# Kernel tuning notes

Measured on AMD Instinct MI355X. Metric: run time of the kernel, lower is better.

The kernel has to match this reference:

```python
import jax, jax.numpy as jnp
import numpy as np

DIM = 2048
N_HEADS = 16
Q_RANK = 1536
KV_RANK = 512
D_NOPE = 128
D_ROPE = 64
D_V = 128
EPS = 1e-6
B, S = 2, 2048
ROPE_THETA = 10000.0


def rmsnorm(x, w, eps=EPS):
    return x * jax.lax.rsqrt(jnp.mean(x * x, axis=-1, keepdims=True) + eps) * w


def apply_rope(x):
    # x: [b, h, s, d] with d even; LLaMA-style interleaved pair rotation
    b, h, s, d = x.shape
    inv_freq = 1.0 / (ROPE_THETA ** (jnp.arange(0, d, 2, dtype=jnp.float32) / d))
    ang = jnp.arange(s, dtype=jnp.float32)[:, None] * inv_freq[None, :]  # [s, d/2]
    cos, sin = jnp.cos(ang), jnp.sin(ang)
    xr = x.reshape(b, h, s, d // 2, 2)
    x1, x2 = xr[..., 0], xr[..., 1]
    o1 = x1 * cos - x2 * sin
    o2 = x1 * sin + x2 * cos
    return jnp.stack([o1, o2], axis=-1).reshape(b, h, s, d)


def setup_inputs() -> dict:
    key = jax.random.key(0)
    ks = jax.random.split(key, 10)
    std = 0.02
    return {
        "x": jax.random.normal(ks[0], (B, S, DIM), dtype=jnp.float32),
        "wq_down": jax.random.normal(ks[1], (Q_RANK, DIM), dtype=jnp.float32) * std,
        "q_norm_w": jnp.ones((Q_RANK,), dtype=jnp.float32),
        "wq_up": jax.random.normal(ks[2], (N_HEADS * D_NOPE, Q_RANK), dtype=jnp.float32) * std,
        "wq_rope": jax.random.normal(ks[3], (N_HEADS * D_ROPE, Q_RANK), dtype=jnp.float32) * std,
        "wkv_down": jax.random.normal(ks[4], (KV_RANK, DIM), dtype=jnp.float32) * std,
        "kv_norm_w": jnp.ones((KV_RANK,), dtype=jnp.float32),
        "wkv_up": jax.random.normal(ks[5], (N_HEADS * (D_NOPE + D_V), KV_RANK), dtype=jnp.float32) * std,
        "wk_rope": jax.random.normal(ks[6], (D_ROPE, DIM), dtype=jnp.float32) * std,
        "wo": jax.random.normal(ks[7], (DIM, N_HEADS * D_V), dtype=jnp.float32) * std,
    }


def reference(x, wq_down, q_norm_w, wq_up, wq_rope, wkv_down, kv_norm_w, wkv_up, wk_rope, wo):
    bs, s, _ = x.shape
    # low-rank Q path
    q_c = rmsnorm(x @ wq_down.T, q_norm_w)                              # [b,s,qr]
    q_nope = (q_c @ wq_up.T).reshape(bs, s, N_HEADS, D_NOPE).transpose(0, 2, 1, 3)
    q_pe = (q_c @ wq_rope.T).reshape(bs, s, N_HEADS, D_ROPE).transpose(0, 2, 1, 3)
    # low-rank KV path
    kv_c = rmsnorm(x @ wkv_down.T, kv_norm_w)                           # [b,s,kvr]
    kv_up = (kv_c @ wkv_up.T).reshape(bs, s, N_HEADS, D_NOPE + D_V)
    k_nope = kv_up[..., :D_NOPE].transpose(0, 2, 1, 3)                  # [b,h,s,dn]
    v = kv_up[..., D_NOPE:].transpose(0, 2, 1, 3)                       # [b,h,s,dv]
    # shared rope key (1 head), broadcast across heads
    k_rope = (x @ wk_rope.T).reshape(bs, s, 1, D_ROPE).transpose(0, 2, 1, 3)  # [b,1,s,dr]
    q_pe = apply_rope(q_pe)
    k_rope = apply_rope(k_rope)
    q = jnp.concatenate([q_nope, q_pe], axis=-1)                        # [b,h,s,dn+dr]
    k = jnp.concatenate([k_nope, jnp.broadcast_to(k_rope, (bs, N_HEADS, s, D_ROPE))], axis=-1)
    scale = 1.0 / np.sqrt(D_NOPE + D_ROPE)
    scores = jnp.einsum('bhqd,bhkd->bhqk', q, k) * scale                # [b,h,s,s]
    causal = jnp.tril(jnp.ones((s, s), dtype=bool))
    scores = jnp.where(causal, scores, -jnp.inf)
    probs = jax.nn.softmax(scores, axis=-1)
    out = jnp.einsum('bhqk,bhkv->bhqv', probs, v)                       # [b,h,s,dv]
    out = out.transpose(0, 2, 1, 3).reshape(bs, s, N_HEADS * D_V)
    return out @ wo.T
```

## Files before the change

### kernel.cpp

```cpp
#include <hip/hip_runtime.h>
#include <stdint.h>

typedef _Float16 f16x8 __attribute__((ext_vector_type(8)));
typedef _Float16 f16x4 __attribute__((ext_vector_type(4)));
typedef float fx4 __attribute__((ext_vector_type(4)));

static constexpr int S_LEN = 2048;
static constexpr int BATCH = 2;
static constexpr int TOKENS = BATCH * S_LEN;
static constexpr int DIM = 2048;
static constexpr int NH = 16;
static constexpr int QR = 1536;
static constexpr int KVR = 512;
static constexpr int DN = 128;
static constexpr int DR = 64;
static constexpr int DV = 128;

__device__ __forceinline__ void async16(const _Float16* g, _Float16* lds_base_uniform) {
  __builtin_amdgcn_global_load_lds(
      (const __attribute__((address_space(1))) void*)g,
      (__attribute__((address_space(3))) void*)lds_base_uniform, 16, 0, 0);
}

__device__ __forceinline__ void bar() {
  asm volatile("" ::: "memory");
  __builtin_amdgcn_s_barrier();
  asm volatile("" ::: "memory");
}
#define VMWAIT(n) asm volatile("s_waitcnt vmcnt(" #n ")" ::: "memory")

#define ROR16(x, ctrl) \
  __uint_as_float(__builtin_amdgcn_update_dpp(__float_as_uint(x), __float_as_uint(x), \
                                              (ctrl), 0xF, 0xF, false))

struct CvtSegs {
  const float* src[8];
  _Float16* dst[8];
  int n4[8];
  int cum[9];
};
__global__ __launch_bounds__(256) void cvt_all(CvtSegs s) {
  const int b = blockIdx.x;
  int seg = 0;
#pragma unroll
  for (int k = 0; k < 7; ++k) seg += (b >= s.cum[seg + 1]) ? 1 : 0;
  const int i = (b - s.cum[seg]) * 256 + threadIdx.x;
  if (i >= s.n4[seg]) return;
  fx4 v = *(const fx4*)(s.src[seg] + (size_t)i * 4);
  f16x4 o;
  o[0] = (_Float16)v[0]; o[1] = (_Float16)v[1];
  o[2] = (_Float16)v[2]; o[3] = (_Float16)v[3];
  *(f16x4*)(s.dst[seg] + (size_t)i * 4) = o;
}

template <int MODE>
__global__ __launch_bounds__(256) void gemm_nt(const _Float16* __restrict__ A,
                                               const _Float16* __restrict__ W,
                                               void* __restrict__ C0v,
                                               void* __restrict__ C1v,
                                               int M, int N, int K) {
  __shared__ __attribute__((aligned(16))) _Float16 As[3][128 * 32];
  __shared__ __attribute__((aligned(16))) _Float16 Ws[3][128 * 32];
  const int tid = threadIdx.x;
  const int lane = tid & 63;
  const int wave = tid >> 6;
  const int wr = (wave >> 1) * 64;
  const int wc = (wave & 1) * 64;
  const int m16 = lane & 15;
  const int quad = lane >> 4;
  const int m0 = blockIdx.y * 128;
  const int n0 = blockIdx.x * 128;

  auto stage = [&](int buf, int k0) {
#pragma unroll
    for (int p = 0; p < 2; ++p) {
      const int cb = p * 256 + wave * 64;
      const int ch = cb + lane;
      const int r = ch >> 2;
      const int c8 = (ch & 3) * 8;
      async16(A + (size_t)(m0 + r) * K + k0 + c8, &As[buf][cb * 8]);
      async16(W + (size_t)(n0 + r) * K + k0 + c8, &Ws[buf][cb * 8]);
    }
  };

  const fx4 fz = {0.f, 0.f, 0.f, 0.f};
  fx4 acc[4][4];
#pragma unroll
  for (int i = 0; i < 4; ++i)
#pragma unroll
    for (int j = 0; j < 4; ++j) acc[i][j] = fz;

  const int nkt = K >> 5;
  stage(0, 0);
  stage(1, 32);
  int cur = 0;
  for (int kt = 0; kt < nkt; ++kt) {
    if (kt + 1 < nkt) { VMWAIT(4); } else { VMWAIT(0); }
    bar();
    if (kt + 2 < nkt) {
      int b2 = cur + 2; if (b2 >= 3) b2 -= 3;
      stage(b2, (kt + 2) * 32);
    }
    const _Float16* as = As[cur];
    const _Float16* ws = Ws[cur];
    f16x8 af[4], wf[4];
#pragma unroll
    for (int i = 0; i < 4; ++i)
      af[i] = *(const f16x8*)(&as[(wr + i * 16 + m16) * 32 + quad * 8]);
#pragma unroll
    for (int j = 0; j < 4; ++j)
      wf[j] = *(const f16x8*)(&ws[(wc + j * 16 + m16) * 32 + quad * 8]);
#pragma unroll
    for (int i = 0; i < 4; ++i)
#pragma unroll
      for (int j = 0; j < 4; ++j)
        acc[i][j] = __builtin_amdgcn_mfma_f32_16x16x32_f16(af[i], wf[j], acc[i][j], 0, 0, 0);
    if (++cur == 3) cur = 0;
  }

#pragma unroll
  for (int j = 0; j < 4; ++j) {
    const int col = n0 + wc + j * 16 + m16;
    if (MODE == 2) {
      _Float16* KN = (_Float16*)C0v;
      _Float16* VT = (_Float16*)C1v;
      const int head = col >> 8;
      const int sub = col & 255;
      if (sub < 128) {
#pragma unroll
        for (int i = 0; i < 4; ++i)
#pragma unroll
          for (int r = 0; r < 4; ++r)
            KN[(size_t)(m0 + wr + i * 16 + quad * 4 + r) * 2048 + head * 128 + sub] =
                (_Float16)acc[i][j][r];
      } else {
        const int dv = sub - 128;
#pragma unroll
        for (int i = 0; i < 4; ++i) {
          f16x4 v;
#pragma unroll
          for (int r = 0; r < 4; ++r) v[r] = (_Float16)acc[i][j][r];
          *(f16x4*)(&VT[(size_t)(head * 128 + dv) * TOKENS + m0 + wr + i * 16 + quad * 4]) = v;
        }
      }
    } else if (MODE == 3) {
#pragma unroll
      for (int i = 0; i < 4; ++i)
#pragma unroll
        for (int r = 0; r < 4; ++r) {
          const size_t row = (size_t)(m0 + wr + i * 16 + quad * 4 + r);
          if (col < 2048) ((_Float16*)C0v)[row * 2048 + col] = (_Float16)acc[i][j][r];
          else ((_Float16*)C1v)[row * 1024 + col - 2048] = (_Float16)acc[i][j][r];
        }
    } else if (MODE == 4) {
      if (col < 576) {
#pragma unroll
        for (int i = 0; i < 4; ++i)
#pragma unroll
          for (int r = 0; r < 4; ++r) {
            const size_t row = (size_t)(m0 + wr + i * 16 + quad * 4 + r);
            if (col < 512) ((_Float16*)C0v)[row * 512 + col] = (_Float16)acc[i][j][r];
            else ((_Float16*)C1v)[row * 64 + col - 512] = (_Float16)acc[i][j][r];
          }
      }
    } else {
      if (col < N) {
#pragma unroll
        for (int i = 0; i < 4; ++i)
#pragma unroll
          for (int r = 0; r < 4; ++r) {
            const size_t row = (size_t)(m0 + wr + i * 16 + quad * 4 + r);
            if (MODE == 0) ((_Float16*)C0v)[row * N + col] = (_Float16)acc[i][j][r];
            else ((float*)C0v)[row * N + col] = acc[i][j][r];
          }
      }
    }
  }
}

template <int NC>
__global__ __launch_bounds__(256) void rmsnorm_ip(_Float16* __restrict__ xx,
                                                  const float* __restrict__ w) {
  const int row = blockIdx.x;
  _Float16* p = xx + (size_t)row * NC;
  float ss = 0.f;
  for (int c = threadIdx.x; c < NC; c += 256) {
    const float v = (float)p[c];
    ss += v * v;
  }
#pragma unroll
  for (int d = 1; d < 64; d <<= 1) ss += __shfl_xor(ss, d);
  __shared__ float red[4];
  if ((threadIdx.x & 63) == 0) red[threadIdx.x >> 6] = ss;
  __syncthreads();
  const float rs = rsqrtf((red[0] + red[1] + red[2] + red[3]) * (1.0f / NC) + 1e-6f);
  for (int c = threadIdx.x; c < NC; c += 256)
    p[c] = (_Float16)((float)p[c] * rs * w[c]);
}

__global__ void rope_q(_Float16* __restrict__ qpe) {
  const int idx = blockIdx.x * 256 + threadIdx.x;
  const int t = idx >> 9;
  const int rem = idx & 511;
  const int hh = rem >> 5;
  const int i = rem & 31;
  const int s = t & (S_LEN - 1);
  const float fr = exp2f(-(float)i * 0.4152410118609203f);
  const float ang = (float)s * fr;
  const float sn = sinf(ang), cs = cosf(ang);
  const size_t base = (size_t)t * (NH * DR) + hh * DR + 2 * i;
  const float x1 = (float)qpe[base];
  const float x2 = (float)qpe[base + 1];
  qpe[base] = (_Float16)(x1 * cs - x2 * sn);
  qpe[base + 1] = (_Float16)(x1 * sn + x2 * cs);
}

__global__ void rope_k(_Float16* __restrict__ kr) {
  const int idx = blockIdx.x * 256 + threadIdx.x;
  const int t = idx >> 5;
  const int i = idx & 31;
  const int s = t & (S_LEN - 1);
  const float fr = exp2f(-(float)i * 0.4152410118609203f);
  const float ang = (float)s * fr;
  const float sn = sinf(ang), cs = cosf(ang);
  const size_t base = (size_t)t * DR + 2 * i;
  const float x1 = (float)kr[base];
  const float x2 = (float)kr[base + 1];
  kr[base] = (_Float16)(x1 * cs - x2 * sn);
  kr[base + 1] = (_Float16)(x1 * sn + x2 * cs);
}

__global__ __launch_bounds__(256, 2) void mla_attn(
    const _Float16* __restrict__ qn,
    const _Float16* __restrict__ qp,
    const _Float16* __restrict__ kn,
    const _Float16* __restrict__ kr,
    const _Float16* __restrict__ vT,
    _Float16* __restrict__ out)
{
  __shared__ __attribute__((aligned(16))) _Float16 Ks[2][768 * 8];
  __shared__ __attribute__((aligned(16))) _Float16 Vs[2][512 * 8];
  __shared__ __attribute__((aligned(16))) _Float16 Ps[4][16][40];

  const int bid = blockIdx.x;
  const int j = bid >> 5;
  const int bh = bid & 31;
  const int b = bh >> 4;
  const int h = bh & 15;
  const int q32 = 31 - j;
  const int qb = q32 * 64;
  const int tok0 = b * S_LEN;

  const int tid = threadIdx.x;
  const int lane = tid & 63;
  const int wave = tid >> 6;
  const int m16 = lane & 15;
  const int quad = lane >> 4;
  const int R0 = qb + wave * 16;

  auto stageKV = [&](int buf, int kbase) {
#pragma unroll
    for (int jj = 0; jj < 3; ++jj) {
      const int i = wave * 3 + jj;
      const int ch = i * 2 + (lane >> 5);
      const int key = lane & 31;
      const _Float16* g = (ch < 16)
          ? kn + (size_t)(tok0 + kbase + key) * 2048 + h * 128 + ch * 8
          : kr + (size_t)(tok0 + kbase + key) * 64 + (ch - 16) * 8;
      async16(g, &Ks[buf][i * 512]);
    }
#pragma unroll
    for (int jj = 0; jj < 2; ++jj) {
      const int i = wave * 2 + jj;
      const int p = i * 64 + lane;
      const int L = p ^ ((p >> 3) & 3);
      const int dv = L >> 2;
      const int qc = L & 3;
      async16(vT + (size_t)(h * 128 + dv) * TOKENS + tok0 + kbase + qc * 8,
              &Vs[buf][i * 512]);
    }
  };

  const float scale2 = 0.07216878364870323f * 1.4426950408889634f;
  const fx4 fz = {0.f, 0.f, 0.f, 0.f};

  f16x8 qf[6];
  {
    const size_t t = (size_t)(tok0 + qb + wave * 16 + m16);
#pragma unroll
    for (int kk = 0; kk < 4; ++kk)
      qf[kk] = *(const f16x8*)(qn + t * 2048 + h * 128 + kk * 32 + quad * 8);
#pragma unroll
    for (int kk = 0; kk < 2; ++kk)
      qf[4 + kk] = *(const f16x8*)(qp + t * 1024 + h * 64 + kk * 32 + quad * 8);
  }

  fx4 oacc[8];
#pragma unroll
  for (int n = 0; n < 8; ++n) oacc[n] = fz;
  float mst[4], lst[4];
#pragma unroll
  for (int r = 0; r < 4; ++r) { mst[r] = -3.0e38f; lst[r] = 0.f; }

  const int nkt = (qb >> 5) + 2;

  stageKV(0, 0);
  for (int kt = 0; kt < nkt; ++kt) {
    const int kbase = kt * 32;
    __syncthreads();
    if (kt + 1 < nkt) stageKV((kt + 1) & 1, kbase + 32);

    const bool live = (kbase <= R0 + 15);
    if (!live) continue;
    const _Float16* ks = Ks[kt & 1];
    const _Float16* vs = Vs[kt & 1];

    fx4 sc[2];
    sc[0] = fz; sc[1] = fz;
    __builtin_amdgcn_s_setprio(1);
#pragma unroll
    for (int kk = 0; kk < 6; ++kk) {
#pragma unroll
      for (int n = 0; n < 2; ++n) {
        f16x8 kf = *(const f16x8*)(&ks[(kk * 128 + quad * 32 + n * 16 + m16) * 8]);
        sc[n] = __builtin_amdgcn_mfma_f32_16x16x32_f16(qf[kk], kf, sc[n], 0, 0, 0);
      }
    }
    __builtin_amdgcn_s_setprio(0);

    f16x8 vf[8];
#pragma unroll
    for (int n8 = 0; n8 < 8; ++n8) {
      const int c0 = (n8 * 16 + m16) * 4 + quad;
      vf[n8] = *(const f16x8*)(&vs[(c0 ^ ((c0 >> 3) & 3)) * 8]);
    }

    const bool needmask = (kbase + 31 > R0);
    float alpha[4];
    bool any_upd = false;
#pragma unroll
    for (int r = 0; r < 4; ++r) {
      float v0 = sc[0][r] * scale2;
      float v1 = sc[1][r] * scale2;
      if (needmask) {
        const int qrow = R0 + quad * 4 + r;
        if (kbase + m16 > qrow)      v0 = -3.0e38f;
        if (kbase + 16 + m16 > qrow) v1 = -3.0e38f;
      }
      float mx = fmaxf(v0, v1);
      mx = fmaxf(mx, ROR16(mx, 0x128));
      mx = fmaxf(mx, ROR16(mx, 0x124));
      mx = fmaxf(mx, ROR16(mx, 0x122));
      mx = fmaxf(mx, ROR16(mx, 0x121));
      float al = 1.0f;
      if (__any(mx > mst[r] + 10.0f)) {
        const float mn = fmaxf(mst[r], mx);
        al = exp2f(mst[r] - mn);
        mst[r] = mn;
        any_upd = true;
      }
      alpha[r] = al;
      const float p0 = exp2f(v0 - mst[r]);
      const float p1 = exp2f(v1 - mst[r]);
      float ls = p0 + p1;
      ls += ROR16(ls, 0x128);
      ls += ROR16(ls, 0x124);
      ls += ROR16(ls, 0x122);
      ls += ROR16(ls, 0x121);
      lst[r] = lst[r] * al + ls;
      _Float16* pr = &Ps[wave][quad * 4 + r][0];
      pr[m16] = (_Float16)p0;
      pr[16 + m16] = (_Float16)p1;
    }
    if (any_upd) {
#pragma unroll
      for (int n8 = 0; n8 < 8; ++n8)
#pragma unroll
        for (int r = 0; r < 4; ++r) oacc[n8][r] *= alpha[r];
    }

    f16x8 pf = *(const f16x8*)(&Ps[wave][m16][quad * 8]);
    __builtin_amdgcn_s_setprio(1);
#pragma unroll
    for (int n8 = 0; n8 < 8; ++n8)
      oacc[n8] = __builtin_amdgcn_mfma_f32_16x16x32_f16(pf, vf[n8], oacc[n8], 0, 0, 0);
    __builtin_amdgcn_s_setprio(0);
  }

  float inv[4];
#pragma unroll
  for (int r = 0; r < 4; ++r) inv[r] = 1.0f / lst[r];
#pragma unroll
  for (int n8 = 0; n8 < 8; ++n8) {
#pragma unroll
    for (int r = 0; r < 4; ++r) {
      const size_t t = (size_t)(tok0 + qb + wave * 16 + quad * 4 + r);
      out[t * 2048 + h * 128 + n8 * 16 + m16] = (_Float16)(oacc[n8][r] * inv[r]);
    }
  }
}

extern "C" void kernel_launch(void* const* d_in, const int* in_sizes, int n_in,
                              void* d_out, int out_size, void* d_ws, size_t ws_size,
                              hipStream_t stream) {
  const float* x         = (const float*)d_in[0];
  const float* wq_down   = (const float*)d_in[1];
  const float* q_norm_w  = (const float*)d_in[2];
  const float* wq_up     = (const float*)d_in[3];
  const float* wq_rope   = (const float*)d_in[4];
  const float* wkv_down  = (const float*)d_in[5];
  const float* kv_norm_w = (const float*)d_in[6];
  const float* wkv_up    = (const float*)d_in[7];
  const float* wk_rope   = (const float*)d_in[8];
  const float* wo        = (const float*)d_in[9];
  float* out = (float*)d_out;

  char* ws = (char*)d_ws;
  size_t off = 0;
  auto alloc = [&](size_t bytes) {
    char* p = ws + off;
    off += (bytes + 255) & ~(size_t)255;
    return p;
  };
  _Float16* x_h     = (_Float16*)alloc((size_t)TOKENS * DIM * 2);
  _Float16* wqd_h   = (_Float16*)alloc((size_t)QR * DIM * 2);
  _Float16* wquqr_h = (_Float16*)alloc((size_t)3072 * QR * 2);
  _Float16* wkvdr_h = (_Float16*)alloc((size_t)576 * DIM * 2);
  _Float16* wkvu_h  = (_Float16*)alloc((size_t)NH * 256 * KVR * 2);
  _Float16* wo_h    = (_Float16*)alloc((size_t)DIM * NH * DV * 2);
  _Float16* qc_h    = (_Float16*)alloc((size_t)TOKENS * QR * 2);
  _Float16* kvc_h   = (_Float16*)alloc((size_t)TOKENS * KVR * 2);
  _Float16* qnope_h = (_Float16*)alloc((size_t)TOKENS * 2048 * 2);
  _Float16* qpe_h   = (_Float16*)alloc((size_t)TOKENS * 1024 * 2);
  _Float16* knope_h = (_Float16*)alloc((size_t)TOKENS * 2048 * 2);
  _Float16* vT_h    = (_Float16*)alloc((size_t)2048 * TOKENS * 2);
  _Float16* krope_h = (_Float16*)alloc((size_t)TOKENS * DR * 2);
  _Float16* attn_h  = (_Float16*)alloc((size_t)TOKENS * 2048 * 2);

  CvtSegs cs;
  const float* srcs[8] = {x, wq_down, wq_up, wq_rope, wkv_down, wk_rope, wkv_up, wo};
  _Float16* dsts[8] = {x_h, wqd_h, wquqr_h, wquqr_h + (size_t)2048 * QR,
                       wkvdr_h, wkvdr_h + (size_t)512 * DIM, wkvu_h, wo_h};
  const size_t ns[8] = {(size_t)TOKENS * DIM, (size_t)QR * DIM, (size_t)2048 * QR,
                        (size_t)1024 * QR, (size_t)KVR * DIM, (size_t)DR * DIM,
                        (size_t)NH * 256 * KVR, (size_t)DIM * NH * DV};
  int cum = 0;
  for (int i = 0; i < 8; ++i) {
    cs.src[i] = srcs[i];
    cs.dst[i] = dsts[i];
    cs.n4[i] = (int)(ns[i] / 4);
    cs.cum[i] = cum;
    cum += (cs.n4[i] + 255) / 256;
  }
  cs.cum[8] = cum;
  cvt_all<<<dim3(cum), 256, 0, stream>>>(cs);

  auto gx = [](int n) { return (unsigned)((n + 127) / 128); };
  const unsigned gm = TOKENS / 128;

  gemm_nt<0><<<dim3(gx(QR), gm), 256, 0, stream>>>(x_h, wqd_h, qc_h, nullptr, TOKENS, QR, DIM);
  rmsnorm_ip<QR><<<dim3(TOKENS), 256, 0, stream>>>(qc_h, q_norm_w);
  gemm_nt<4><<<dim3(gx(576), gm), 256, 0, stream>>>(x_h, wkvdr_h, kvc_h, krope_h, TOKENS, 576, DIM);
  rmsnorm_ip<KVR><<<dim3(TOKENS), 256, 0, stream>>>(kvc_h, kv_norm_w);
  rope_k<<<dim3(TOKENS * 32 / 256), 256, 0, stream>>>(krope_h);
  gemm_nt<3><<<dim3(gx(3072), gm), 256, 0, stream>>>(qc_h, wquqr_h, qnope_h, qpe_h, TOKENS, 3072, QR);
  rope_q<<<dim3(TOKENS * NH * 32 / 256), 256, 0, stream>>>(qpe_h);
  gemm_nt<2><<<dim3(gx(4096), gm), 256, 0, stream>>>(kvc_h, wkvu_h, knope_h, vT_h, TOKENS, 4096, KVR);
  mla_attn<<<dim3(1024), 256, 0, stream>>>(qnope_h, qpe_h, knope_h, krope_h, vT_h, attn_h);
  gemm_nt<1><<<dim3(gx(DIM), gm), 256, 0, stream>>>(attn_h, wo_h, out, nullptr, TOKENS, DIM, NH * DV);
}
```

Baseline: 512.4 us.

## Merge down-projections, fuse norms and rope, fold q-rope and row-sum into attention

Concatenates the wq_down, wkv_down and wk_rope weights so a single GEMM produces q_c, kv_c and k_rope. The two rmsnorms and rope_k become one launch, and the two up-projection GEMMs become one launch dispatched by block index. The q rope is applied in registers while Q is loaded inside attention, and the softmax denominator is now taken from an extra MFMA against a ones vector instead of DPP reductions; sin/cos use hardware revolution-based intrinsics. This removes several launches and a global read-write pass over q_pe, at the cost of an extra MFMA per tile and lower-precision trig.

```diff
diff --git a/kernel.cpp b/kernel.cpp
--- a/kernel.cpp
+++ b/kernel.cpp
@@ -33,6 +33,13 @@
   __uint_as_float(__builtin_amdgcn_update_dpp(__float_as_uint(x), __float_as_uint(x), \
                                               (ctrl), 0xF, 0xF, false))
 
+__device__ __forceinline__ void sincos_rev(float ang, float* sn, float* cs) {
+  float rev = ang * 0.15915494309189535f;
+  rev -= floorf(rev);
+  *sn = __builtin_amdgcn_sinf(rev);
+  *cs = __builtin_amdgcn_cosf(rev);
+}
+
 struct CvtSegs {
   const float* src[8];
   _Float16* dst[8];
@@ -58,6 +65,7 @@
                                                const _Float16* __restrict__ W,
                                                void* __restrict__ C0v,
                                                void* __restrict__ C1v,
+                                               void* __restrict__ C2v,
                                                int M, int N, int K) {
   __shared__ __attribute__((aligned(16))) _Float16 As[3][128 * 32];
   __shared__ __attribute__((aligned(16))) _Float16 Ws[3][128 * 32];
@@ -121,9 +129,112 @@
 #pragma unroll
   for (int j = 0; j < 4; ++j) {
     const int col = n0 + wc + j * 16 + m16;
-    if (MODE == 2) {
-      _Float16* KN = (_Float16*)C0v;
-      _Float16* VT = (_Float16*)C1v;
+    if (MODE == 5) {
+#pragma unroll
+      for (int i = 0; i < 4; ++i)
+#pragma unroll
+        for (int r = 0; r < 4; ++r) {
+          const size_t row = (size_t)(m0 + wr + i * 16 + quad * 4 + r);
+          const _Float16 v = (_Float16)acc[i][j][r];
+          if (col < 1536)      ((_Float16*)C0v)[row * 1536 + col] = v;
+          else if (col < 2048) ((_Float16*)C1v)[row * 512 + col - 1536] = v;
+          else if (col < 2112) ((_Float16*)C2v)[row * 64 + col - 2048] = v;
+        }
+    } else {
+      if (col < N) {
+#pragma unroll
+        for (int i = 0; i < 4; ++i)
+#pragma unroll
+          for (int r = 0; r < 4; ++r) {
+            const size_t row = (size_t)(m0 + wr + i * 16 + quad * 4 + r);
+            ((float*)C0v)[row * N + col] = acc[i][j][r];
+          }
+      }
+    }
+  }
+}
+
+__global__ __launch_bounds__(256) void gemm_up(
+    const _Float16* __restrict__ qc, const _Float16* __restrict__ wqu,
+    const _Float16* __restrict__ kvc, const _Float16* __restrict__ wkvu,
+    _Float16* __restrict__ qnope, _Float16* __restrict__ qpe,
+    _Float16* __restrict__ knope, _Float16* __restrict__ vT) {
+  __shared__ __attribute__((aligned(16))) _Float16 As[3][128 * 32];
+  __shared__ __attribute__((aligned(16))) _Float16 Ws[3][128 * 32];
+  const int tid = threadIdx.x;
+  const int lane = tid & 63;
+  const int wave = tid >> 6;
+  const int wr = (wave >> 1) * 64;
+  const int wc = (wave & 1) * 64;
+  const int m16 = lane & 15;
+  const int quad = lane >> 4;
+  const int m0 = blockIdx.y * 128;
+  const bool isq = (blockIdx.x < 24);
+  const int n0 = (isq ? blockIdx.x : blockIdx.x - 24) * 128;
+  const _Float16* A = isq ? qc : kvc;
+  const _Float16* W = isq ? wqu : wkvu;
+  const int K = isq ? QR : KVR;
+
+  auto stage = [&](int buf, int k0) {
+#pragma unroll
+    for (int p = 0; p < 2; ++p) {
+      const int cb = p * 256 + wave * 64;
+      const int ch = cb + lane;
+      const int r = ch >> 2;
+      const int c8 = (ch & 3) * 8;
+      async16(A + (size_t)(m0 + r) * K + k0 + c8, &As[buf][cb * 8]);
+      async16(W + (size_t)(n0 + r) * K + k0 + c8, &Ws[buf][cb * 8]);
+    }
+  };
+
+  const fx4 fz = {0.f, 0.f, 0.f, 0.f};
+  fx4 acc[4][4];
+#pragma unroll
+  for (int i = 0; i < 4; ++i)
+#pragma unroll
+    for (int j = 0; j < 4; ++j) acc[i][j] = fz;
+
+  const int nkt = K >> 5;
+  stage(0, 0);
+  stage(1, 32);
+  int cur = 0;
+  for (int kt = 0; kt < nkt; ++kt) {
+    if (kt + 1 < nkt) { VMWAIT(4); } else { VMWAIT(0); }
+    bar();
+    if (kt + 2 < nkt) {
+      int b2 = cur + 2; if (b2 >= 3) b2 -= 3;
+      stage(b2, (kt + 2) * 32);
+    }
+    const _Float16* as = As[cur];
+    const _Float16* ws = Ws[cur];
+    f16x8 af[4], wf[4];
+#pragma unroll
+    for (int i = 0; i < 4; ++i)
+      af[i] = *(const f16x8*)(&as[(wr + i * 16 + m16) * 32 + quad * 8]);
+#pragma unroll
+    for (int j = 0; j < 4; ++j)
+      wf[j] = *(const f16x8*)(&ws[(wc + j * 16 + m16) * 32 + quad * 8]);
+#pragma unroll
+    for (int i = 0; i < 4; ++i)
+#pragma unroll
+      for (int j = 0; j < 4; ++j)
+        acc[i][j] = __builtin_amdgcn_mfma_f32_16x16x32_f16(af[i], wf[j], acc[i][j], 0, 0, 0);
+    if (++cur == 3) cur = 0;
+  }
+
+#pragma unroll
+  for (int j = 0; j < 4; ++j) {
+    const int col = n0 + wc + j * 16 + m16;
+    if (isq) {
+#pragma unroll
+      for (int i = 0; i < 4; ++i)
+#pragma unroll
+        for (int r = 0; r < 4; ++r) {
+          const size_t row = (size_t)(m0 + wr + i * 16 + quad * 4 + r);
+          if (col < 2048) qnope[row * 2048 + col] = (_Float16)acc[i][j][r];
+          else qpe[row * 1024 + col - 2048] = (_Float16)acc[i][j][r];
+        }
+    } else {
       const int head = col >> 8;
       const int sub = col & 255;
       if (sub < 128) {
@@ -131,7 +242,7 @@
         for (int i = 0; i < 4; ++i)
 #pragma unroll
           for (int r = 0; r < 4; ++r)
-            KN[(size_t)(m0 + wr + i * 16 + quad * 4 + r) * 2048 + head * 128 + sub] =
+            knope[(size_t)(m0 + wr + i * 16 + quad * 4 + r) * 2048 + head * 128 + sub] =
                 (_Float16)acc[i][j][r];
       } else {
         const int dv = sub - 128;
@@ -140,94 +251,53 @@
           f16x4 v;
 #pragma unroll
           for (int r = 0; r < 4; ++r) v[r] = (_Float16)acc[i][j][r];
-          *(f16x4*)(&VT[(size_t)(head * 128 + dv) * TOKENS + m0 + wr + i * 16 + quad * 4]) = v;
+          *(f16x4*)(&vT[(size_t)(head * 128 + dv) * TOKENS + m0 + wr + i * 16 + quad * 4]) = v;
         }
       }
-    } else if (MODE == 3) {
-#pragma unroll
-      for (int i = 0; i < 4; ++i)
-#pragma unroll
-        for (int r = 0; r < 4; ++r) {
-          const size_t row = (size_t)(m0 + wr + i * 16 + quad * 4 + r);
-          if (col < 2048) ((_Float16*)C0v)[row * 2048 + col] = (_Float16)acc[i][j][r];
-          else ((_Float16*)C1v)[row * 1024 + col - 2048] = (_Float16)acc[i][j][r];
-        }
-    } else if (MODE == 4) {
-      if (col < 576) {
-#pragma unroll
-        for (int i = 0; i < 4; ++i)
-#pragma unroll
-          for (int r = 0; r < 4; ++r) {
-            const size_t row = (size_t)(m0 + wr + i * 16 + quad * 4 + r);
-            if (col < 512) ((_Float16*)C0v)[row * 512 + col] = (_Float16)acc[i][j][r];
-            else ((_Float16*)C1v)[row * 64 + col - 512] = (_Float16)acc[i][j][r];
-          }
-      }
-    } else {
-      if (col < N) {
-#pragma unroll
-        for (int i = 0; i < 4; ++i)
-#pragma unroll
-          for (int r = 0; r < 4; ++r) {
-            const size_t row = (size_t)(m0 + wr + i * 16 + quad * 4 + r);
-            if (MODE == 0) ((_Float16*)C0v)[row * N + col] = (_Float16)acc[i][j][r];
-            else ((float*)C0v)[row * N + col] = acc[i][j][r];
-          }
-      }
-    }
-  }
-}
-
-template <int NC>
-__global__ __launch_bounds__(256) void rmsnorm_ip(_Float16* __restrict__ xx,
-                                                  const float* __restrict__ w) {
-  const int row = blockIdx.x;
-  _Float16* p = xx + (size_t)row * NC;
-  float ss = 0.f;
-  for (int c = threadIdx.x; c < NC; c += 256) {
-    const float v = (float)p[c];
-    ss += v * v;
-  }
-#pragma unroll
-  for (int d = 1; d < 64; d <<= 1) ss += __shfl_xor(ss, d);
-  __shared__ float red[4];
-  if ((threadIdx.x & 63) == 0) red[threadIdx.x >> 6] = ss;
-  __syncthreads();
-  const float rs = rsqrtf((red[0] + red[1] + red[2] + red[3]) * (1.0f / NC) + 1e-6f);
-  for (int c = threadIdx.x; c < NC; c += 256)
-    p[c] = (_Float16)((float)p[c] * rs * w[c]);
-}
-
-__global__ void rope_q(_Float16* __restrict__ qpe) {
-  const int idx = blockIdx.x * 256 + threadIdx.x;
-  const int t = idx >> 9;
-  const int rem = idx & 511;
-  const int hh = rem >> 5;
-  const int i = rem & 31;
-  const int s = t & (S_LEN - 1);
-  const float fr = exp2f(-(float)i * 0.4152410118609203f);
-  const float ang = (float)s * fr;
-  const float sn = sinf(ang), cs = cosf(ang);
-  const size_t base = (size_t)t * (NH * DR) + hh * DR + 2 * i;
-  const float x1 = (float)qpe[base];
-  const float x2 = (float)qpe[base + 1];
-  qpe[base] = (_Float16)(x1 * cs - x2 * sn);
-  qpe[base + 1] = (_Float16)(x1 * sn + x2 * cs);
-}
-
-__global__ void rope_k(_Float16* __restrict__ kr) {
-  const int idx = blockIdx.x * 256 + threadIdx.x;
-  const int t = idx >> 5;
-  const int i = idx & 31;
-  const int s = t & (S_LEN - 1);
-  const float fr = exp2f(-(float)i * 0.4152410118609203f);
-  const float ang = (float)s * fr;
-  const float sn = sinf(ang), cs = cosf(ang);
-  const size_t base = (size_t)t * DR + 2 * i;
-  const float x1 = (float)kr[base];
-  const float x2 = (float)kr[base + 1];
-  kr[base] = (_Float16)(x1 * cs - x2 * sn);
-  kr[base + 1] = (_Float16)(x1 * sn + x2 * cs);
+    }
+  }
+}
+
+__global__ __launch_bounds__(256) void rms_rope(_Float16* __restrict__ qc,
+                                                const float* __restrict__ qw,
+                                                _Float16* __restrict__ kvc,
+                                                const float* __restrict__ kvw,
+                                                _Float16* __restrict__ kr) {
+  const int bid = blockIdx.x;
+  if (bid < 2 * TOKENS) {
+    const bool isq = bid < TOKENS;
+    const int row = isq ? bid : bid - TOKENS;
+    const int NC = isq ? QR : KVR;
+    _Float16* p = (isq ? qc : kvc) + (size_t)row * NC;
+    const float* w = isq ? qw : kvw;
+    float ss = 0.f;
+    for (int c = threadIdx.x; c < NC; c += 256) {
+      const float v = (float)p[c];
+      ss += v * v;
+    }
+#pragma unroll
+    for (int d = 1; d < 64; d <<= 1) ss += __shfl_xor(ss, d);
+    __shared__ float red[4];
+    if ((threadIdx.x & 63) == 0) red[threadIdx.x >> 6] = ss;
+    __syncthreads();
+    const float rs = rsqrtf((red[0] + red[1] + red[2] + red[3]) / (float)NC + 1e-6f);
+    for (int c = threadIdx.x; c < NC; c += 256)
+      p[c] = (_Float16)((float)p[c] * rs * w[c]);
+  } else {
+    const int idx = (bid - 2 * TOKENS) * 256 + threadIdx.x;
+    const int t = idx >> 5;
+    const int i = idx & 31;
+    const int s = t & (S_LEN - 1);
+    const float fr = exp2f(-(float)i * 0.4152410118609203f);
+    const float ang = (float)s * fr;
+    float sn, cs;
+    sincos_rev(ang, &sn, &cs);
+    const size_t base = (size_t)t * DR + 2 * i;
+    const float x1 = (float)kr[base];
+    const float x2 = (float)kr[base + 1];
+    kr[base] = (_Float16)(x1 * cs - x2 * sn);
+    kr[base + 1] = (_Float16)(x1 * sn + x2 * cs);
+  }
 }
 
 __global__ __launch_bounds__(256, 2) void mla_attn(
@@ -286,21 +356,38 @@
 
   f16x8 qf[6];
   {
-    const size_t t = (size_t)(tok0 + qb + wave * 16 + m16);
+    const int srow = qb + wave * 16 + m16;
+    const size_t t = (size_t)(tok0 + srow);
 #pragma unroll
     for (int kk = 0; kk < 4; ++kk)
       qf[kk] = *(const f16x8*)(qn + t * 2048 + h * 128 + kk * 32 + quad * 8);
 #pragma unroll
-    for (int kk = 0; kk < 2; ++kk)
-      qf[4 + kk] = *(const f16x8*)(qp + t * 1024 + h * 64 + kk * 32 + quad * 8);
-  }
-
-  fx4 oacc[8];
-#pragma unroll
-  for (int n = 0; n < 8; ++n) oacc[n] = fz;
-  float mst[4], lst[4];
-#pragma unroll
-  for (int r = 0; r < 4; ++r) { mst[r] = -3.0e38f; lst[r] = 0.f; }
+    for (int kk = 0; kk < 2; ++kk) {
+      f16x8 v = *(const f16x8*)(qp + t * 1024 + h * 64 + kk * 32 + quad * 8);
+      f16x8 o;
+      const int i0 = kk * 16 + quad * 4;
+#pragma unroll
+      for (int jj = 0; jj < 4; ++jj) {
+        const float ang = (float)srow * exp2f(-(float)(i0 + jj) * 0.4152410118609203f);
+        float sn, cs;
+        sincos_rev(ang, &sn, &cs);
+        const float x1 = (float)v[2 * jj], x2 = (float)v[2 * jj + 1];
+        o[2 * jj]     = (_Float16)(x1 * cs - x2 * sn);
+        o[2 * jj + 1] = (_Float16)(x1 * sn + x2 * cs);
+      }
+      qf[4 + kk] = o;
+    }
+  }
+
+  fx4 oacc[9];
+#pragma unroll
+  for (int n = 0; n < 9; ++n) oacc[n] = fz;
+  float mst[4];
+#pragma unroll
+  for (int r = 0; r < 4; ++r) mst[r] = -3.0e38f;
+  f16x8 vones;
+#pragma unroll
+  for (int e = 0; e < 8; ++e) vones[e] = (_Float16)1.0f;
 
   const int nkt = (qb >> 5) + 2;
 
@@ -347,13 +434,14 @@
         if (kbase + m16 > qrow)      v0 = -3.0e38f;
         if (kbase + 16 + m16 > qrow) v1 = -3.0e38f;
       }
-      float mx = fmaxf(v0, v1);
-      mx = fmaxf(mx, ROR16(mx, 0x128));
-      mx = fmaxf(mx, ROR16(mx, 0x124));
-      mx = fmaxf(mx, ROR16(mx, 0x122));
-      mx = fmaxf(mx, ROR16(mx, 0x121));
+      const float pre = fmaxf(v0, v1);
       float al = 1.0f;
-      if (__any(mx > mst[r] + 10.0f)) {
+      if (__any(pre > mst[r] + 10.0f)) {
+        float mx = pre;
+        mx = fmaxf(mx, ROR16(mx, 0x128));
+        mx = fmaxf(mx, ROR16(mx, 0x124));
+        mx = fmaxf(mx, ROR16(mx, 0x122));
+        mx = fmaxf(mx, ROR16(mx, 0x121));
         const float mn = fmaxf(mst[r], mx);
         al = exp2f(mst[r] - mn);
         mst[r] = mn;
@@ -362,19 +450,13 @@
       alpha[r] = al;
       const float p0 = exp2f(v0 - mst[r]);
       const float p1 = exp2f(v1 - mst[r]);
-      float ls = p0 + p1;
-      ls += ROR16(ls, 0x128);
-      ls += ROR16(ls, 0x124);
-      ls += ROR16(ls, 0x122);
-      ls += ROR16(ls, 0x121);
-      lst[r] = lst[r] * al + ls;
       _Float16* pr = &Ps[wave][quad * 4 + r][0];
       pr[m16] = (_Float16)p0;
       pr[16 + m16] = (_Float16)p1;
     }
     if (any_upd) {
 #pragma unroll
-      for (int n8 = 0; n8 < 8; ++n8)
+      for (int n8 = 0; n8 < 9; ++n8)
 #pragma unroll
         for (int r = 0; r < 4; ++r) oacc[n8][r] *= alpha[r];
     }
@@ -384,12 +466,13 @@
 #pragma unroll
     for (int n8 = 0; n8 < 8; ++n8)
       oacc[n8] = __builtin_amdgcn_mfma_f32_16x16x32_f16(pf, vf[n8], oacc[n8], 0, 0, 0);
+    oacc[8] = __builtin_amdgcn_mfma_f32_16x16x32_f16(pf, vones, oacc[8], 0, 0, 0);
     __builtin_amdgcn_s_setprio(0);
   }
 
   float inv[4];
 #pragma unroll
-  for (int r = 0; r < 4; ++r) inv[r] = 1.0f / lst[r];
+  for (int r = 0; r < 4; ++r) inv[r] = 1.0f / oacc[8][r];
 #pragma unroll
   for (int n8 = 0; n8 < 8; ++n8) {
 #pragma unroll
@@ -423,9 +506,8 @@
     return p;
   };
   _Float16* x_h     = (_Float16*)alloc((size_t)TOKENS * DIM * 2);
-  _Float16* wqd_h   = (_Float16*)alloc((size_t)QR * DIM * 2);
+  _Float16* wA_h    = (_Float16*)alloc((size_t)2176 * DIM * 2);
   _Float16* wquqr_h = (_Float16*)alloc((size_t)3072 * QR * 2);
-  _Float16* wkvdr_h = (_Float16*)alloc((size_t)576 * DIM * 2);
   _Float16* wkvu_h  = (_Float16*)alloc((size_t)NH * 256 * KVR * 2);
   _Float16* wo_h    = (_Float16*)alloc((size_t)DIM * NH * DV * 2);
   _Float16* qc_h    = (_Float16*)alloc((size_t)TOKENS * QR * 2);
@@ -439,8 +521,9 @@
 
   CvtSegs cs;
   const float* srcs[8] = {x, wq_down, wq_up, wq_rope, wkv_down, wk_rope, wkv_up, wo};
-  _Float16* dsts[8] = {x_h, wqd_h, wquqr_h, wquqr_h + (size_t)2048 * QR,
-                       wkvdr_h, wkvdr_h + (size_t)512 * DIM, wkvu_h, wo_h};
+  _Float16* dsts[8] = {x_h, wA_h, wquqr_h, wquqr_h + (size_t)2048 * QR,
+                       wA_h + (size_t)1536 * DIM, wA_h + (size_t)2048 * DIM,
+                       wkvu_h, wo_h};
   const size_t ns[8] = {(size_t)TOKENS * DIM, (size_t)QR * DIM, (size_t)2048 * QR,
                         (size_t)1024 * QR, (size_t)KVR * DIM, (size_t)DR * DIM,
                         (size_t)NH * 256 * KVR, (size_t)DIM * NH * DV};
@@ -455,17 +538,15 @@
   cs.cum[8] = cum;
   cvt_all<<<dim3(cum), 256, 0, stream>>>(cs);
 
-  auto gx = [](int n) { return (unsigned)((n + 127) / 128); };
   const unsigned gm = TOKENS / 128;
 
-  gemm_nt<0><<<dim3(gx(QR), gm), 256, 0, stream>>>(x_h, wqd_h, qc_h, nullptr, TOKENS, QR, DIM);
-  rmsnorm_ip<QR><<<dim3(TOKENS), 256, 0, stream>>>(qc_h, q_norm_w);
-  gemm_nt<4><<<dim3(gx(576), gm), 256, 0, stream>>>(x_h, wkvdr_h, kvc_h, krope_h, TOKENS, 576, DIM);
-  rmsnorm_ip<KVR><<<dim3(TOKENS), 256, 0, stream>>>(kvc_h, kv_norm_w);
-  rope_k<<<dim3(TOKENS * 32 / 256), 256, 0, stream>>>(krope_h);
-  gemm_nt<3><<<dim3(gx(3072), gm), 256, 0, stream>>>(qc_h, wquqr_h, qnope_h, qpe_h, TOKENS, 3072, QR);
-  rope_q<<<dim3(TOKENS * NH * 32 / 256), 256, 0, stream>>>(qpe_h);
-  gemm_nt<2><<<dim3(gx(4096), gm), 256, 0, stream>>>(kvc_h, wkvu_h, knope_h, vT_h, TOKENS, 4096, KVR);
+  gemm_nt<5><<<dim3(17, gm), 256, 0, stream>>>(x_h, wA_h, qc_h, kvc_h, krope_h,
+                                               TOKENS, 2112, DIM);
+  rms_rope<<<dim3(2 * TOKENS + TOKENS * 32 / 256), 256, 0, stream>>>(
+      qc_h, q_norm_w, kvc_h, kv_norm_w, krope_h);
+  gemm_up<<<dim3(24 + 32, gm), 256, 0, stream>>>(qc_h, wquqr_h, kvc_h, wkvu_h,
+                                                 qnope_h, qpe_h, knope_h, vT_h);
   mla_attn<<<dim3(1024), 256, 0, stream>>>(qnope_h, qpe_h, knope_h, krope_h, vT_h, attn_h);
-  gemm_nt<1><<<dim3(gx(DIM), gm), 256, 0, stream>>>(attn_h, wo_h, out, nullptr, TOKENS, DIM, NH * DV);
-}
+  gemm_nt<1><<<dim3(16, gm), 256, 0, stream>>>(attn_h, wo_h, out, nullptr, nullptr,
+                                               TOKENS, DIM, NH * DV);
+}
```

After: 475.8 us. 7.1% less time.
